# Optimization experiments

Measured on AMD Instinct MI355X. Metric: run time of the kernel, lower is better.

## Reference

```python
import jax, jax.numpy as jnp
import numpy as np

E = 768   # embed_size
H = 64    # head_embed_size
B = 8
T = 4096  # == ctx_size


def setup_inputs() -> dict:
    key = jax.random.key(0)
    k1, k2, k3, k4 = jax.random.split(key, 4)
    inputs = jax.random.normal(k1, (B, T, E), dtype=jnp.float32)
    # Linear weights stored as (E, H) so projection is x @ W
    scale = 1.0 / np.sqrt(E)
    Wq = jax.random.uniform(k2, (E, H), dtype=jnp.float32, minval=-scale, maxval=scale)
    Wk = jax.random.uniform(k3, (E, H), dtype=jnp.float32, minval=-scale, maxval=scale)
    Wv = jax.random.uniform(k4, (E, H), dtype=jnp.float32, minval=-scale, maxval=scale)
    return {"inputs": inputs, "Wq": Wq, "Wk": Wk, "Wv": Wv}


def reference(inputs, Wq, Wk, Wv):
    Tlen = inputs.shape[1]
    q = inputs @ Wq  # (B,T,H)
    k = inputs @ Wk  # (B,T,H)
    v = inputs @ Wv  # (B,T,H)
    # NOTE: original module does NOT scale by 1/sqrt(H) — faithful reproduction.
    scores = jnp.einsum('bqh,bkh->bqk', q, k)  # (B,T,T)
    causal = jnp.tril(jnp.ones((Tlen, Tlen), dtype=bool))
    scores = jnp.where(causal, scores, -jnp.inf)
    attn = jax.nn.softmax(scores, axis=-1)
    # dropout=0 -> identity
    out = jnp.einsum('bqk,bkh->bqh', attn, v)  # (B,T,H)
    return out
```

## Files before the change

kernel.cpp:

```cpp
#include <hip/hip_runtime.h>
#include <hip/hip_bf16.h>

#define E_DIM 768
#define H_DIM 64
#define B_SZ 8
#define T_SZ 4096
#define BT (B_SZ * T_SZ)

typedef __attribute__((ext_vector_type(8))) short short8;
typedef __attribute__((ext_vector_type(4))) short bf16x4;
typedef __attribute__((ext_vector_type(4))) float floatx4;

#define RAWBAR() __asm__ volatile("s_waitcnt lgkmcnt(0)\n\ts_barrier" ::: "memory")

static __device__ __forceinline__ unsigned short bf1(float a) {
    __hip_bfloat16 h = __float2bfloat16(a);
    unsigned short u; __builtin_memcpy(&u, &h, 2); return u;
}
static __device__ __forceinline__ unsigned int pk2(float a, float b) {
    __hip_bfloat162 h = __float22bfloat162_rn(float2{a, b});
    unsigned int u; __builtin_memcpy(&u, &h, 4); return u;
}

__global__ __launch_bounds__(256) void prep_w(
    const float* __restrict__ Wq, const float* __restrict__ Wk,
    const float* __restrict__ Wv, unsigned short* __restrict__ Wt)
{
    __shared__ float Ls[64][65];
    const int nt = blockIdx.x;
    const int kc = blockIdx.y;
    const float* __restrict__ W = (nt == 0) ? Wq : (nt == 1) ? Wk : Wv;
    const float scl = (nt == 0) ? 1.44269504088896f : 1.0f;
    const int t = threadIdx.x;
    const int k0 = kc * 64;

#pragma unroll
    for (int it = 0; it < 16; ++it) {
        const int kk = (t >> 6) + it * 4;
        Ls[kk][t & 63] = W[(size_t)(k0 + kk) * H_DIM + (t & 63)];
    }
    __syncthreads();

#pragma unroll
    for (int it = 0; it < 4; ++it) {
        const int nl = (t >> 4) + it * 16;
        const int kl = (t & 15) * 4;
        unsigned int u[2];
        u[0] = pk2(Ls[kl + 0][nl] * scl, Ls[kl + 1][nl] * scl);
        u[1] = pk2(Ls[kl + 2][nl] * scl, Ls[kl + 3][nl] * scl);
        *(uint2*)(Wt + (size_t)(nt * 64 + nl) * E_DIM + k0 + kl) = *(uint2*)u;
    }
}

__global__ __launch_bounds__(768) void proj_mfma(
    const float* __restrict__ X, const unsigned short* __restrict__ Wt,
    unsigned short* __restrict__ Qb, unsigned short* __restrict__ Kb,
    unsigned short* __restrict__ Vtb)
{
    __shared__ unsigned short Xs[2][16][776];

    const int tid  = threadIdx.x;
    const int wave = tid >> 6, lane = tid & 63;
    const int row  = lane & 15, quad = lane >> 4;
    const int m0   = blockIdx.x * 128;

    short8 bfr[24];
    {
        const unsigned short* wp = Wt + (size_t)(wave * 16 + row) * E_DIM + quad * 8;
#pragma unroll
        for (int ks = 0; ks < 24; ++ks) bfr[ks] = *(const short8*)(wp + ks * 32);
    }

    const int srow = tid & 15;
    const int sc   = tid >> 4;
    const float* __restrict__ xbase = X + (size_t)(m0 + srow) * E_DIM + sc * 16;

    float4 fx[4];
#define LDX(mt)                                                               \
    {                                                                         \
        const float* p = xbase + (size_t)(mt) * 16 * E_DIM;                   \
        fx[0] = *(const float4*)(p);     fx[1] = *(const float4*)(p + 4);     \
        fx[2] = *(const float4*)(p + 8); fx[3] = *(const float4*)(p + 12);    \
    }
#define STX(buf)                                                              \
    {                                                                         \
        unsigned int tmp[8];                                                  \
        tmp[0] = pk2(fx[0].x, fx[0].y); tmp[1] = pk2(fx[0].z, fx[0].w);       \
        tmp[2] = pk2(fx[1].x, fx[1].y); tmp[3] = pk2(fx[1].z, fx[1].w);       \
        tmp[4] = pk2(fx[2].x, fx[2].y); tmp[5] = pk2(fx[2].z, fx[2].w);       \
        tmp[6] = pk2(fx[3].x, fx[3].y); tmp[7] = pk2(fx[3].z, fx[3].w);       \
        *(int4*)&Xs[buf][srow][sc * 16]     = *(int4*)&tmp[0];                \
        *(int4*)&Xs[buf][srow][sc * 16 + 8] = *(int4*)&tmp[4];                \
    }

    LDX(0); STX(0); LDX(1);
    RAWBAR();

    const int g  = wave >> 2;
    const int h  = (wave & 3) * 16 + row;
    unsigned short* __restrict__ OQK = (g == 0) ? Qb : Kb;
    const int bb = m0 >> 12;

    int cur = 0;
    for (int mt = 0; mt < 8; ++mt) {
        if (mt < 7) STX(cur ^ 1);
        if (mt < 6) LDX(mt + 2);

        floatx4 a0 = (floatx4)0.0f, a1 = (floatx4)0.0f;
        floatx4 a2 = (floatx4)0.0f, a3 = (floatx4)0.0f;
#pragma unroll
        for (int ks = 0; ks < 6; ++ks) {
            const short8 f0 = *(const short8*)&Xs[cur][row][(ks * 4 + 0) * 32 + quad * 8];
            const short8 f1 = *(const short8*)&Xs[cur][row][(ks * 4 + 1) * 32 + quad * 8];
            const short8 f2 = *(const short8*)&Xs[cur][row][(ks * 4 + 2) * 32 + quad * 8];
            const short8 f3 = *(const short8*)&Xs[cur][row][(ks * 4 + 3) * 32 + quad * 8];
            a0 = __builtin_amdgcn_mfma_f32_16x16x32_bf16(f0, bfr[ks * 4 + 0], a0, 0, 0, 0);
            a1 = __builtin_amdgcn_mfma_f32_16x16x32_bf16(f1, bfr[ks * 4 + 1], a1, 0, 0, 0);
            a2 = __builtin_amdgcn_mfma_f32_16x16x32_bf16(f2, bfr[ks * 4 + 2], a2, 0, 0, 0);
            a3 = __builtin_amdgcn_mfma_f32_16x16x32_bf16(f3, bfr[ks * 4 + 3], a3, 0, 0, 0);
        }
        floatx4 acc;
#pragma unroll
        for (int r = 0; r < 4; ++r) acc[r] = (a0[r] + a1[r]) + (a2[r] + a3[r]);

        const int mr = m0 + mt * 16 + quad * 4;
        if (g < 2) {
#pragma unroll
            for (int r = 0; r < 4; ++r)
                OQK[(size_t)(mr + r) * H_DIM + h] = bf1(acc[r]);
        } else {
            const int t0 = mr & 4095;
            unsigned int u[2];
            u[0] = pk2(acc[0], acc[1]); u[1] = pk2(acc[2], acc[3]);
            *(uint2*)(Vtb + ((size_t)bb * H_DIM + h) * T_SZ + t0) = *(uint2*)u;
        }

        RAWBAR();
        cur ^= 1;
    }
#undef LDX
#undef STX
}

__global__ __launch_bounds__(256, 6) void attn_mfma(
    const unsigned short* __restrict__ Qb,
    const unsigned short* __restrict__ Kb,
    const unsigned short* __restrict__ Vtb,
    float* __restrict__ Opart, float* __restrict__ lpart,
    float* __restrict__ Out)
{
    __shared__ __align__(16) unsigned short KV[2][64][72];
    __shared__ float lc[4][16];

    const int lb   = blockIdx.x;
    const int b    = lb & 7;
    const int s    = lb >> 3;
    const bool split = (s < 128);
    const int qq   = split ? (127 - (s >> 1)) : (191 - s);
    const int half = s & 1;
    const int nkt_tot = (qq >> 1) + 1;
    const int hsp  = (nkt_tot + 1) >> 1;
    const int k0t  = (split && half) ? hsp : 0;
    const int k1t  = (split && !half) ? hsp : nkt_tot;
    const int ktd  = nkt_tot - 1;
    const int n    = k1t - k0t;

    const int tid  = threadIdx.x;
    const int wave = tid >> 6, lane = tid & 63;
    const int col  = lane & 15, quad = lane >> 4;
    const int wq   = wave >> 1;
    const int wk   = wave & 1;

    const size_t base = (size_t)b * T_SZ * H_DIM;
    const int q0  = qq * 32;

    short8 qf0, qf1;
    {
        const unsigned short* qp = Qb + base + (size_t)(q0 + wq * 16 + col) * H_DIM + quad * 8;
        qf0 = *(const short8*)(qp);
        qf1 = *(const short8*)(qp + 32);
    }

    floatx4 o[4];
#pragma unroll
    for (int i = 0; i < 4; ++i) o[i] = (floatx4)0.0f;
    float lp = 0.0f;

    const int krow = tid >> 2, kcol = (tid & 3) * 16;
    const unsigned short* __restrict__ Ksrc = Kb + base + (size_t)krow * H_DIM + kcol;
    const unsigned short* __restrict__ Vsrc = Vtb + ((size_t)b * H_DIM + krow) * T_SZ + kcol;

    int4 kr0, kr1, vr0, vr1;
#define LDKV(t)                                                          \
    {                                                                    \
        const unsigned short* kp = Ksrc + (size_t)(t) * 64 * H_DIM;      \
        kr0 = *(const int4*)kp; kr1 = *(const int4*)(kp + 8);            \
        const unsigned short* vp = Vsrc + (t) * 64;                      \
        vr0 = *(const int4*)vp; vr1 = *(const int4*)(vp + 8);            \
    }
#define STKV()                                                           \
    {                                                                    \
        *(int4*)&KV[0][krow][kcol] = kr0; *(int4*)&KV[0][krow][kcol + 8] = kr1; \
        *(int4*)&KV[1][krow][kcol] = vr0; *(int4*)&KV[1][krow][kcol + 8] = vr1; \
    }

    LDKV(k0t);
    STKV();
    if (n > 1) LDKV(k0t + 1);
    RAWBAR();

    for (int i = 0; i < n; ++i) {
        const int kt = k0t + i;

        floatx4 sv[2];
        __builtin_amdgcn_s_setprio(1);
#pragma unroll
        for (int j = 0; j < 2; ++j) {
            const unsigned short* kp = &KV[0][wk * 32 + j * 16 + col][quad * 8];
            floatx4 a = (floatx4)0.0f;
            a = __builtin_amdgcn_mfma_f32_16x16x32_bf16(*(const short8*)(kp),      qf0, a, 0, 0, 0);
            a = __builtin_amdgcn_mfma_f32_16x16x32_bf16(*(const short8*)(kp + 32), qf1, a, 0, 0, 0);
            sv[j] = a;
        }
        __builtin_amdgcn_s_setprio(0);

        if (kt == ktd) {
            const int qg = q0 + wq * 16 + col;
#pragma unroll
            for (int j = 0; j < 2; ++j) {
                const int kb0 = kt * 64 + wk * 32 + j * 16 + quad * 4;
#pragma unroll
                for (int r = 0; r < 4; ++r)
                    if (kb0 + r > qg) sv[j][r] = -1e30f;
            }
        }

        bf16x4 pa[2];
#pragma unroll
        for (int j = 0; j < 2; ++j) {
            float p0 = exp2f(fminf(sv[j][0], 110.0f));
            float p1 = exp2f(fminf(sv[j][1], 110.0f));
            float p2 = exp2f(fminf(sv[j][2], 110.0f));
            float p3 = exp2f(fminf(sv[j][3], 110.0f));
            lp += (p0 + p1) + (p2 + p3);
            unsigned int u0, u1;
            __asm__("v_cvt_pk_bf16_f32 %0, %1, %2" : "=v"(u0) : "v"(p0), "v"(p1));
            __asm__("v_cvt_pk_bf16_f32 %0, %1, %2" : "=v"(u1) : "v"(p2), "v"(p3));
            union { unsigned int u[2]; bf16x4 v; } pu;
            pu.u[0] = u0; pu.u[1] = u1;
            pa[j] = pu.v;
        }

        __builtin_amdgcn_s_setprio(1);
#pragma unroll
        for (int d = 0; d < 4; ++d) {
#pragma unroll
            for (int j = 0; j < 2; ++j) {
                const bf16x4 vb = *(const bf16x4*)(&KV[1][d * 16 + col][wk * 32 + j * 16 + quad * 4]);
                o[d] = __builtin_amdgcn_mfma_f32_16x16x16bf16_1k(pa[j], vb, o[d], 0, 0, 0);
            }
        }
        __builtin_amdgcn_s_setprio(0);

        RAWBAR();
        if (i + 1 < n) {
            STKV();
            if (i + 2 < n) LDKV(kt + 2);
        }
        RAWBAR();
    }

    lp += __shfl_xor(lp, 16);
    lp += __shfl_xor(lp, 32);
    if (quad == 0) lc[wave][col] = lp;
    __syncthreads();

    float* __restrict__ Oc = (float*)&KV[0][0][0];
#pragma unroll
    for (int r = 0; r < 4; ++r)
#pragma unroll
        for (int d = 0; d < 4; ++d)
            Oc[((wave * 16) + quad * 4 + r) * 64 + d * 16 + col] = o[d][r];
    __syncthreads();

    {
        const int orow = tid >> 3;
        const int d0   = (tid & 7) * 8;
        const int rl   = orow & 15;
        const int wb   = (orow >> 4) * 2;
        const float* p0 = &Oc[((wb * 16) + rl) * 64 + d0];
        const float* p1 = &Oc[(((wb + 1) * 16) + rl) * 64 + d0];
        const float lsum = lc[wb][rl] + lc[wb + 1][rl];
        float4 a0 = *(const float4*)(p0);
        float4 a1 = *(const float4*)(p0 + 4);
        const float4 b0 = *(const float4*)(p1);
        const float4 b1 = *(const float4*)(p1 + 4);
        a0.x += b0.x; a0.y += b0.y; a0.z += b0.z; a0.w += b0.w;
        a1.x += b1.x; a1.y += b1.y; a1.z += b1.z; a1.w += b1.w;
        if (!split) {
            const float inv = 1.0f / lsum;
            a0.x *= inv; a0.y *= inv; a0.z *= inv; a0.w *= inv;
            a1.x *= inv; a1.y *= inv; a1.z *= inv; a1.w *= inv;
            float* op = Out + base + (size_t)(q0 + orow) * H_DIM + d0;
            *(float4*)(op)     = a0;
            *(float4*)(op + 4) = a1;
        } else {
            const int pidx = (b * 64 + (qq - 64)) * 2 + half;
            float* op = Opart + ((size_t)pidx * 32 + orow) * 64 + d0;
            *(float4*)(op)     = a0;
            *(float4*)(op + 4) = a1;
            if ((tid & 7) == 0) lpart[pidx * 32 + orow] = lsum;
        }
    }
#undef LDKV
#undef STKV
}

__global__ __launch_bounds__(256) void attn_combine(
    const float* __restrict__ Opart, const float* __restrict__ lpart,
    float* __restrict__ Out)
{
    const int c   = blockIdx.x;
    const int b   = c >> 6;
    const int qi  = c & 63;
    const int qq  = 64 + qi;
    const int tid = threadIdx.x;
    const int orow = tid >> 3;
    const int d0   = (tid & 7) * 8;
    const int p0   = (b * 64 + qi) * 2;

    const float* P0 = Opart + ((size_t)p0 * 32 + orow) * 64 + d0;
    const float* P1 = P0 + 32 * 64;
    const float inv = 1.0f / (lpart[p0 * 32 + orow] + lpart[(p0 + 1) * 32 + orow]);

    float4 a0 = *(const float4*)(P0);
    float4 a1 = *(const float4*)(P0 + 4);
    const float4 b0 = *(const float4*)(P1);
    const float4 b1 = *(const float4*)(P1 + 4);
    a0.x = (a0.x + b0.x) * inv; a0.y = (a0.y + b0.y) * inv;
    a0.z = (a0.z + b0.z) * inv; a0.w = (a0.w + b0.w) * inv;
    a1.x = (a1.x + b1.x) * inv; a1.y = (a1.y + b1.y) * inv;
    a1.z = (a1.z + b1.z) * inv; a1.w = (a1.w + b1.w) * inv;

    float* op = Out + ((size_t)b * T_SZ + qq * 32 + orow) * H_DIM + d0;
    *(float4*)(op)     = a0;
    *(float4*)(op + 4) = a1;
}

extern "C" void kernel_launch(void* const* d_in, const int* in_sizes, int n_in,
                              void* d_out, int out_size, void* d_ws, size_t ws_size,
                              hipStream_t stream) {
    const float* X  = (const float*)d_in[0];
    const float* Wq = (const float*)d_in[1];
    const float* Wk = (const float*)d_in[2];
    const float* Wv = (const float*)d_in[3];

    unsigned short* Wt  = (unsigned short*)d_ws;
    unsigned short* Qb  = Wt + (size_t)192 * E_DIM;
    unsigned short* Kb  = Qb + (size_t)BT * H_DIM;
    unsigned short* Vtb = Kb + (size_t)BT * H_DIM;
    float* Opart = (float*)(Vtb + (size_t)BT * H_DIM);
    float* lpart = Opart + (size_t)1024 * 32 * 64;

    prep_w<<<dim3(3, 12), 256, 0, stream>>>(Wq, Wk, Wv, Wt);
    proj_mfma<<<256, 768, 0, stream>>>(X, Wt, Qb, Kb, Vtb);
    attn_mfma<<<1536, 256, 0, stream>>>(Qb, Kb, Vtb, Opart, lpart, (float*)d_out);
    attn_combine<<<512, 256, 0, stream>>>(Opart, lpart, (float*)d_out);
}
```

Baseline: 219.9 us.

## Load K/V fragments directly from global into registers, dropping LDS staging

The attention kernel no longer stages K and V tiles through shared memory with barriers. Each wave loads its own MFMA fragments straight from global memory into registers, double-buffered across iterations. K rows are permuted so the QK^T output layout feeds PV directly as a 16x16x32 bf16 operand, replacing the eight 16x16x16 MFMAs per tile with four. Occupancy hint drops from 6 to 4 waves per SIMD to make room for the larger register footprint. The cost is redundant global/L2 traffic, since both wave rows load the same K/V, and higher register pressure.

```diff
diff --git a/kernel.cpp b/kernel.cpp
--- a/kernel.cpp
+++ b/kernel.cpp
@@ -8,7 +8,6 @@
 #define BT (B_SZ * T_SZ)
 
 typedef __attribute__((ext_vector_type(8))) short short8;
-typedef __attribute__((ext_vector_type(4))) short bf16x4;
 typedef __attribute__((ext_vector_type(4))) float floatx4;
 
 #define RAWBAR() __asm__ volatile("s_waitcnt lgkmcnt(0)\n\ts_barrier" ::: "memory")
@@ -142,14 +141,14 @@
 #undef STX
 }
 
-__global__ __launch_bounds__(256, 6) void attn_mfma(
+__global__ __launch_bounds__(256, 4) void attn_mfma(
     const unsigned short* __restrict__ Qb,
     const unsigned short* __restrict__ Kb,
     const unsigned short* __restrict__ Vtb,
     float* __restrict__ Opart, float* __restrict__ lpart,
     float* __restrict__ Out)
 {
-    __shared__ __align__(16) unsigned short KV[2][64][72];
+    __shared__ float Oc[4 * 16 * 64];
     __shared__ float lc[4][16];
 
     const int lb   = blockIdx.x;
@@ -186,96 +185,89 @@
     for (int i = 0; i < 4; ++i) o[i] = (floatx4)0.0f;
     float lp = 0.0f;
 
-    const int krow = tid >> 2, kcol = (tid & 3) * 16;
-    const unsigned short* __restrict__ Ksrc = Kb + base + (size_t)krow * H_DIM + kcol;
-    const unsigned short* __restrict__ Vsrc = Vtb + ((size_t)b * H_DIM + krow) * T_SZ + kcol;
-
-    int4 kr0, kr1, vr0, vr1;
-#define LDKV(t)                                                          \
-    {                                                                    \
-        const unsigned short* kp = Ksrc + (size_t)(t) * 64 * H_DIM;      \
-        kr0 = *(const int4*)kp; kr1 = *(const int4*)(kp + 8);            \
-        const unsigned short* vp = Vsrc + (t) * 64;                      \
-        vr0 = *(const int4*)vp; vr1 = *(const int4*)(vp + 8);            \
-    }
-#define STKV()                                                           \
-    {                                                                    \
-        *(int4*)&KV[0][krow][kcol] = kr0; *(int4*)&KV[0][krow][kcol + 8] = kr1; \
-        *(int4*)&KV[1][krow][kcol] = vr0; *(int4*)&KV[1][krow][kcol + 8] = vr1; \
-    }
-
-    LDKV(k0t);
-    STKV();
-    if (n > 1) LDKV(k0t + 1);
-    RAWBAR();
-
-    for (int i = 0; i < n; ++i) {
-        const int kt = k0t + i;
-
-        floatx4 sv[2];
-        __builtin_amdgcn_s_setprio(1);
-#pragma unroll
-        for (int j = 0; j < 2; ++j) {
-            const unsigned short* kp = &KV[0][wk * 32 + j * 16 + col][quad * 8];
-            floatx4 a = (floatx4)0.0f;
-            a = __builtin_amdgcn_mfma_f32_16x16x32_bf16(*(const short8*)(kp),      qf0, a, 0, 0, 0);
-            a = __builtin_amdgcn_mfma_f32_16x16x32_bf16(*(const short8*)(kp + 32), qf1, a, 0, 0, 0);
-            sv[j] = a;
-        }
-        __builtin_amdgcn_s_setprio(0);
-
-        if (kt == ktd) {
-            const int qg = q0 + wq * 16 + col;
-#pragma unroll
-            for (int j = 0; j < 2; ++j) {
-                const int kb0 = kt * 64 + wk * 32 + j * 16 + quad * 4;
-#pragma unroll
-                for (int r = 0; r < 4; ++r)
-                    if (kb0 + r > qg) sv[j][r] = -1e30f;
-            }
-        }
-
-        bf16x4 pa[2];
-#pragma unroll
-        for (int j = 0; j < 2; ++j) {
-            float p0 = exp2f(fminf(sv[j][0], 110.0f));
-            float p1 = exp2f(fminf(sv[j][1], 110.0f));
-            float p2 = exp2f(fminf(sv[j][2], 110.0f));
-            float p3 = exp2f(fminf(sv[j][3], 110.0f));
-            lp += (p0 + p1) + (p2 + p3);
-            unsigned int u0, u1;
-            __asm__("v_cvt_pk_bf16_f32 %0, %1, %2" : "=v"(u0) : "v"(p0), "v"(p1));
-            __asm__("v_cvt_pk_bf16_f32 %0, %1, %2" : "=v"(u1) : "v"(p2), "v"(p3));
-            union { unsigned int u[2]; bf16x4 v; } pu;
-            pu.u[0] = u0; pu.u[1] = u1;
-            pa[j] = pu.v;
-        }
-
-        __builtin_amdgcn_s_setprio(1);
-#pragma unroll
-        for (int d = 0; d < 4; ++d) {
-#pragma unroll
-            for (int j = 0; j < 2; ++j) {
-                const bf16x4 vb = *(const bf16x4*)(&KV[1][d * 16 + col][wk * 32 + j * 16 + quad * 4]);
-                o[d] = __builtin_amdgcn_mfma_f32_16x16x16bf16_1k(pa[j], vb, o[d], 0, 0, 0);
-            }
-        }
-        __builtin_amdgcn_s_setprio(0);
-
-        RAWBAR();
-        if (i + 1 < n) {
-            STKV();
-            if (i + 2 < n) LDKV(kt + 2);
-        }
-        RAWBAR();
-    }
+    const unsigned short* __restrict__ Kp0 =
+        Kb + base + (size_t)(wk * 32 + ((col >> 2) * 8) + (col & 3)) * H_DIM + quad * 8;
+    const unsigned short* __restrict__ Vp =
+        Vtb + ((size_t)b * H_DIM + col) * T_SZ + wk * 32 + quad * 8;
+
+    short8 kf0[4], vf0[4], kf1[4], vf1[4];
+
+#define LDT(S, t)                                                             \
+    {                                                                         \
+        const unsigned short* kp = Kp0 + (size_t)(t) * 4096;                  \
+        kf##S[0] = *(const short8*)(kp);                                      \
+        kf##S[1] = *(const short8*)(kp + 32);                                 \
+        kf##S[2] = *(const short8*)(kp + 256);              \
+        kf##S[3] = *(const short8*)(kp + 256 + 32);                           \
+        const unsigned short* vp = Vp + (t) * 64;                             \
+        vf##S[0] = *(const short8*)(vp);                                      \
+        vf##S[1] = *(const short8*)(vp + 16 * T_SZ);                          \
+        vf##S[2] = *(const short8*)(vp + 32 * T_SZ);                          \
+        vf##S[3] = *(const short8*)(vp + 48 * T_SZ);                          \
+    }
+
+#define COMP(S, kt)                                                           \
+    {                                                                         \
+        floatx4 a0 = (floatx4)0.0f, a1 = (floatx4)0.0f;                       \
+        __builtin_amdgcn_s_setprio(1);                                        \
+        a0 = __builtin_amdgcn_mfma_f32_16x16x32_bf16(kf##S[0], qf0, a0, 0, 0, 0); \
+        a0 = __builtin_amdgcn_mfma_f32_16x16x32_bf16(kf##S[1], qf1, a0, 0, 0, 0); \
+        a1 = __builtin_amdgcn_mfma_f32_16x16x32_bf16(kf##S[2], qf0, a1, 0, 0, 0); \
+        a1 = __builtin_amdgcn_mfma_f32_16x16x32_bf16(kf##S[3], qf1, a1, 0, 0, 0); \
+        __builtin_amdgcn_s_setprio(0);                                        \
+        if ((kt) == ktd) {                         \
+            const int qg = q0 + wq * 16 + col;                                \
+            const int kb0 = (kt) * 64 + wk * 32 + quad * 8;                   \
+            _Pragma("unroll")                                                 \
+            for (int r = 0; r < 4; ++r) {                                     \
+                if (kb0 + r > qg)     a0[r] = -1e30f;                         \
+                if (kb0 + 4 + r > qg) a1[r] = -1e30f;                         \
+            }                                                                 \
+        }                                                                     \
+        const float p0 = exp2f(fminf(a0[0], 110.0f));                         \
+        const float p1 = exp2f(fminf(a0[1], 110.0f));                         \
+        const float p2 = exp2f(fminf(a0[2], 110.0f));                         \
+        const float p3 = exp2f(fminf(a0[3], 110.0f));                         \
+        const float p4 = exp2f(fminf(a1[0], 110.0f));                         \
+        const float p5 = exp2f(fminf(a1[1], 110.0f));                         \
+        const float p6 = exp2f(fminf(a1[2], 110.0f));                         \
+        const float p7 = exp2f(fminf(a1[3], 110.0f));                         \
+        lp += ((p0 + p1) + (p2 + p3)) + ((p4 + p5) + (p6 + p7));              \
+        unsigned int u0, u1, u2, u3;                                          \
+        __asm__("v_cvt_pk_bf16_f32 %0, %1, %2" : "=v"(u0) : "v"(p0), "v"(p1)); \
+        __asm__("v_cvt_pk_bf16_f32 %0, %1, %2" : "=v"(u1) : "v"(p2), "v"(p3)); \
+        __asm__("v_cvt_pk_bf16_f32 %0, %1, %2" : "=v"(u2) : "v"(p4), "v"(p5)); \
+        __asm__("v_cvt_pk_bf16_f32 %0, %1, %2" : "=v"(u3) : "v"(p6), "v"(p7)); \
+        union { unsigned int u[4]; short8 v; } pu;                            \
+        pu.u[0] = u0; pu.u[1] = u1; pu.u[2] = u2; pu.u[3] = u3;               \
+        const short8 pa = pu.v;                                               \
+        __builtin_amdgcn_s_setprio(1);                                        \
+        o[0] = __builtin_amdgcn_mfma_f32_16x16x32_bf16(pa, vf##S[0], o[0], 0, 0, 0); \
+        o[1] = __builtin_amdgcn_mfma_f32_16x16x32_bf16(pa, vf##S[1], o[1], 0, 0, 0); \
+        o[2] = __builtin_amdgcn_mfma_f32_16x16x32_bf16(pa, vf##S[2], o[2], 0, 0, 0); \
+        o[3] = __builtin_amdgcn_mfma_f32_16x16x32_bf16(pa, vf##S[3], o[3], 0, 0, 0); \
+        __builtin_amdgcn_s_setprio(0);                                        \
+    }
+
+    LDT(0, k0t);
+    if (n > 1) LDT(1, k0t + 1);
+
+    int i = 0;
+    while (true) {
+        COMP(0, k0t + i);
+        if (i + 2 < n) LDT(0, k0t + i + 2);
+        if (++i >= n) break;
+        COMP(1, k0t + i);
+        if (i + 2 < n) LDT(1, k0t + i + 2);
+        if (++i >= n) break;
+    }
+#undef LDT
+#undef COMP
 
     lp += __shfl_xor(lp, 16);
     lp += __shfl_xor(lp, 32);
     if (quad == 0) lc[wave][col] = lp;
-    __syncthreads();
-
-    float* __restrict__ Oc = (float*)&KV[0][0][0];
+
 #pragma unroll
     for (int r = 0; r < 4; ++r)
 #pragma unroll
@@ -312,8 +304,6 @@
             if ((tid & 7) == 0) lpart[pidx * 32 + orow] = lsum;
         }
     }
-#undef LDKV
-#undef STKV
 }
 
 __global__ __launch_bounds__(256) void attn_combine(
```

Measured after the change: 297.5 us. 35.3% more time.

## Split causal attention KV range into up to four chunks for load balance

Applied to the files above, without the earlier changes.

Replaces the two-way KV split for the upper half of query tiles with a graded split: the longest query tiles get four chunks, then three, then two, and the shortest get one. This raises the grid from 1536 to 2560 blocks and evens out per-block work so the tail of the causal triangle idles fewer CUs. The combine kernel now sums a variable number of partials, at the cost of more partial-buffer traffic. It also drops the fminf clamp before exp2f, which removes an instruction but risks overflow for large unscaled scores.

```diff
diff --git a/kernel.cpp b/kernel.cpp
--- a/kernel.cpp
+++ b/kernel.cpp
@@ -152,18 +152,20 @@
     __shared__ __align__(16) unsigned short KV[2][64][72];
     __shared__ float lc[4][16];
 
-    const int lb   = blockIdx.x;
-    const int b    = lb & 7;
-    const int s    = lb >> 3;
-    const bool split = (s < 128);
-    const int qq   = split ? (127 - (s >> 1)) : (191 - s);
-    const int half = s & 1;
-    const int nkt_tot = (qq >> 1) + 1;
-    const int hsp  = (nkt_tot + 1) >> 1;
-    const int k0t  = (split && half) ? hsp : 0;
-    const int k1t  = (split && !half) ? hsp : nkt_tot;
-    const int ktd  = nkt_tot - 1;
+    const int lb = blockIdx.x;
+    const int b  = lb & 7;
+    const int s  = lb >> 3;
+    int qq, c, m;
+    if (s < 128)      { m = 4; qq = 96 + (s >> 2); c = s & 3; }
+    else if (s < 224) { m = 3; const int t = s - 128; const int t3 = t / 3; qq = 64 + t3; c = t - t3 * 3; }
+    else if (s < 288) { m = 2; const int t = s - 224; qq = 32 + (t >> 1); c = t & 1; }
+    else              { m = 1; qq = s - 288; c = 0; }
+    const int ntot = (qq >> 1) + 1;
+    const int k0t  = (c * ntot) / m;
+    const int k1t  = ((c + 1) * ntot) / m;
+    const int ktd  = ntot - 1;
     const int n    = k1t - k0t;
+    const bool split = (m > 1);
 
     const int tid  = threadIdx.x;
     const int wave = tid >> 6, lane = tid & 63;
@@ -238,10 +240,10 @@
         bf16x4 pa[2];
 #pragma unroll
         for (int j = 0; j < 2; ++j) {
-            float p0 = exp2f(fminf(sv[j][0], 110.0f));
-            float p1 = exp2f(fminf(sv[j][1], 110.0f));
-            float p2 = exp2f(fminf(sv[j][2], 110.0f));
-            float p3 = exp2f(fminf(sv[j][3], 110.0f));
+            float p0 = exp2f(sv[j][0]);
+            float p1 = exp2f(sv[j][1]);
+            float p2 = exp2f(sv[j][2]);
+            float p3 = exp2f(sv[j][3]);
             lp += (p0 + p1) + (p2 + p3);
             unsigned int u0, u1;
             __asm__("v_cvt_pk_bf16_f32 %0, %1, %2" : "=v"(u0) : "v"(p0), "v"(p1));
@@ -305,7 +307,7 @@
             *(float4*)(op)     = a0;
             *(float4*)(op + 4) = a1;
         } else {
-            const int pidx = (b * 64 + (qq - 64)) * 2 + half;
+            const int pidx = (b * 96 + (qq - 32)) * 4 + c;
             float* op = Opart + ((size_t)pidx * 32 + orow) * 64 + d0;
             *(float4*)(op)     = a0;
             *(float4*)(op + 4) = a1;
@@ -320,27 +322,28 @@
     const float* __restrict__ Opart, const float* __restrict__ lpart,
     float* __restrict__ Out)
 {
-    const int c   = blockIdx.x;
-    const int b   = c >> 6;
-    const int qi  = c & 63;
-    const int qq  = 64 + qi;
+    const int qi  = blockIdx.x;
+    const int b   = blockIdx.y;
+    const int qq  = 32 + qi;
+    const int m   = (qq < 64) ? 2 : (qq < 96) ? 3 : 4;
     const int tid = threadIdx.x;
     const int orow = tid >> 3;
     const int d0   = (tid & 7) * 8;
-    const int p0   = (b * 64 + qi) * 2;
-
-    const float* P0 = Opart + ((size_t)p0 * 32 + orow) * 64 + d0;
-    const float* P1 = P0 + 32 * 64;
-    const float inv = 1.0f / (lpart[p0 * 32 + orow] + lpart[(p0 + 1) * 32 + orow]);
-
-    float4 a0 = *(const float4*)(P0);
-    float4 a1 = *(const float4*)(P0 + 4);
-    const float4 b0 = *(const float4*)(P1);
-    const float4 b1 = *(const float4*)(P1 + 4);
-    a0.x = (a0.x + b0.x) * inv; a0.y = (a0.y + b0.y) * inv;
-    a0.z = (a0.z + b0.z) * inv; a0.w = (a0.w + b0.w) * inv;
-    a1.x = (a1.x + b1.x) * inv; a1.y = (a1.y + b1.y) * inv;
-    a1.z = (a1.z + b1.z) * inv; a1.w = (a1.w + b1.w) * inv;
+    const int p0   = (b * 96 + qi) * 4;
+
+    float4 a0 = {0.f, 0.f, 0.f, 0.f}, a1 = {0.f, 0.f, 0.f, 0.f};
+    float l = 0.0f;
+    for (int j = 0; j < m; ++j) {
+        const float* P = Opart + ((size_t)(p0 + j) * 32 + orow) * 64 + d0;
+        const float4 b0 = *(const float4*)(P);
+        const float4 b1 = *(const float4*)(P + 4);
+        a0.x += b0.x; a0.y += b0.y; a0.z += b0.z; a0.w += b0.w;
+        a1.x += b1.x; a1.y += b1.y; a1.z += b1.z; a1.w += b1.w;
+        l += lpart[(p0 + j) * 32 + orow];
+    }
+    const float inv = 1.0f / l;
+    a0.x *= inv; a0.y *= inv; a0.z *= inv; a0.w *= inv;
+    a1.x *= inv; a1.y *= inv; a1.z *= inv; a1.w *= inv;
 
     float* op = Out + ((size_t)b * T_SZ + qq * 32 + orow) * H_DIM + d0;
     *(float4*)(op)     = a0;
@@ -360,10 +363,10 @@
     unsigned short* Kb  = Qb + (size_t)BT * H_DIM;
     unsigned short* Vtb = Kb + (size_t)BT * H_DIM;
     float* Opart = (float*)(Vtb + (size_t)BT * H_DIM);
-    float* lpart = Opart + (size_t)1024 * 32 * 64;
+    float* lpart = Opart + (size_t)3072 * 32 * 64;
 
     prep_w<<<dim3(3, 12), 256, 0, stream>>>(Wq, Wk, Wv, Wt);
     proj_mfma<<<256, 768, 0, stream>>>(X, Wt, Qb, Kb, Vtb);
-    attn_mfma<<<1536, 256, 0, stream>>>(Qb, Kb, Vtb, Opart, lpart, (float*)d_out);
-    attn_combine<<<512, 256, 0, stream>>>(Opart, lpart, (float*)d_out);
-}
+    attn_mfma<<<2560, 256, 0, stream>>>(Qb, Kb, Vtb, Opart, lpart, (float*)d_out);
+    attn_combine<<<dim3(96, 8), 256, 0, stream>>>(Opart, lpart, (float*)d_out);
+}
```

Result: no change. 218.1 us (-0.8%).
